# Kernel optimization log

Measured on AMD Instinct MI355X. Metric: run time of the kernel, lower is better.

## Reference

```python
import jax, jax.numpy as jnp
import numpy as np

B, CF, CG, CI = 2, 64, 64, 32
D = H = W = 64

def setup_inputs() -> dict:
    key = jax.random.key(0)
    k1, k2, k3, k4, k5 = jax.random.split(key, 5)
    x = jax.random.normal(k1, (B, CF, D, H, W), dtype=jnp.float32)
    g = jax.random.normal(k2, (B, CG, D, H, W), dtype=jnp.float32)
    # 1x1x1 conv weights reduce to [out_ch, in_ch]; kaiming-like scale
    Wg = jax.random.normal(k3, (CI, CG), dtype=jnp.float32) * (1.0 / np.sqrt(CG))
    Wx = jax.random.normal(k4, (CI, CF), dtype=jnp.float32) * (1.0 / np.sqrt(CF))
    Wpsi = jax.random.normal(k5, (1, CI), dtype=jnp.float32) * (1.0 / np.sqrt(CI))
    return {"x": x, "g": g, "Wg": Wg, "Wx": Wx, "Wpsi": Wpsi}

def reference(x, g, Wg, Wx, Wpsi):
    # 1x1x1 Conv3d == per-voxel matmul over channel dim
    g1 = jnp.einsum('oc,bcdhw->bodhw', Wg, g)          # [B,CI,D,H,W]
    x1 = jnp.einsum('oc,bcdhw->bodhw', Wx, x)          # [B,CI,D,H,W]
    a = jax.nn.relu(g1 + x1)
    psi = jnp.einsum('oc,bcdhw->bodhw', Wpsi, a)       # [B,1,D,H,W]
    psi = jax.nn.sigmoid(psi)
    return x * psi                                      # broadcast over CF
```

## Files before the change

kernel.cpp:

```cpp
#include <hip/hip_runtime.h>


#define SPAT 262144
#define NVOX 524288
#define CIN  64
#define COUT 32

__global__ __launch_bounds__(256) void transpose_w(const float* __restrict__ Wg,
                                                   const float* __restrict__ Wx,
                                                   float* __restrict__ Wcat) {
    int idx = blockIdx.x * 256 + threadIdx.x;
    int c = idx >> 6;
    int o = idx & 63;
    float v = (o < 32) ? Wg[o * CIN + c] : Wx[(o - 32) * CIN + c];
    Wcat[c * 64 + o] = v;
}

__global__ __launch_bounds__(256) void gate_main(const float* __restrict__ x,
                                                 const float* __restrict__ g,
                                                 const float* __restrict__ Wcat,
                                                 const float* __restrict__ Wpsi,
                                                 float* __restrict__ out) {
    int v = blockIdx.x * 256 + threadIdx.x;
    int b = v >> 18;
    int s = v & (SPAT - 1);

    const float* __restrict__ xp = x + (size_t)b * CIN * SPAT + s;
    const float* __restrict__ gp = g + (size_t)b * CIN * SPAT + s;

    float acc[COUT];
#pragma unroll
    for (int o = 0; o < COUT; ++o) acc[o] = 0.0f;

#pragma unroll 4
    for (int c = 0; c < CIN; ++c) {
        float gc = gp[(size_t)c * SPAT];
        float xc = xp[(size_t)c * SPAT];
        const float* w = Wcat + c * 64;
#pragma unroll
        for (int o = 0; o < COUT; ++o)
            acc[o] = fmaf(w[o], gc, fmaf(w[32 + o], xc, acc[o]));
    }

    float p = 0.0f;
#pragma unroll
    for (int o = 0; o < COUT; ++o)
        p = fmaf(Wpsi[o], fmaxf(acc[o], 0.0f), p);

    float psi = 1.0f / (1.0f + __expf(-p));

    float* __restrict__ op = out + (size_t)b * CIN * SPAT + s;
#pragma unroll 4
    for (int c = 0; c < CIN; ++c)
        op[(size_t)c * SPAT] = xp[(size_t)c * SPAT] * psi;
}

extern "C" void kernel_launch(void* const* d_in, const int* in_sizes, int n_in,
                              void* d_out, int out_size, void* d_ws, size_t ws_size,
                              hipStream_t stream) {
    const float* x    = (const float*)d_in[0];
    const float* g    = (const float*)d_in[1];
    const float* Wg   = (const float*)d_in[2];
    const float* Wx   = (const float*)d_in[3];
    const float* Wpsi = (const float*)d_in[4];
    float* out  = (float*)d_out;
    float* Wcat = (float*)d_ws;

    transpose_w<<<16, 256, 0, stream>>>(Wg, Wx, Wcat);
    gate_main<<<NVOX / 256, 256, 0, stream>>>(x, g, Wcat, Wpsi, out);
}
```

Measured before the change: 340.2 us.

## Process two voxels per thread with float2 loads and nontemporal g/out accesses

Each thread now handles two adjacent voxels, using 8-byte vector loads and stores, and reuses each weight load for two voxels. Loads of g and stores of out are marked nontemporal so they do not displace x from cache, since x is re-read in the output pass. Launch bounds request 4 blocks per CU. In exchange each thread holds twice as many accumulators (64 floats), which raises register pressure and may reduce occupancy.

```diff
diff --git a/kernel.cpp b/kernel.cpp
--- a/kernel.cpp
+++ b/kernel.cpp
@@ -5,6 +5,9 @@
 #define NVOX 524288
 #define CIN  64
 #define COUT 32
+#define S2   (SPAT / 2)
+
+typedef float v2f __attribute__((ext_vector_type(2)));
 
 __global__ __launch_bounds__(256) void transpose_w(const float* __restrict__ Wg,
                                                    const float* __restrict__ Wx,
@@ -16,43 +19,52 @@
     Wcat[c * 64 + o] = v;
 }
 
-__global__ __launch_bounds__(256) void gate_main(const float* __restrict__ x,
-                                                 const float* __restrict__ g,
-                                                 const float* __restrict__ Wcat,
-                                                 const float* __restrict__ Wpsi,
-                                                 float* __restrict__ out) {
-    int v = blockIdx.x * 256 + threadIdx.x;
-    int b = v >> 18;
-    int s = v & (SPAT - 1);
+__global__ __launch_bounds__(256, 4) void gate_main(const v2f* __restrict__ x,
+                                                    const v2f* __restrict__ g,
+                                                    const float* __restrict__ Wcat,
+                                                    const float* __restrict__ Wpsi,
+                                                    v2f* __restrict__ out) {
+    int p = blockIdx.x * 256 + threadIdx.x;
+    int b = p >> 17;
+    int s = p & (S2 - 1);
 
-    const float* __restrict__ xp = x + (size_t)b * CIN * SPAT + s;
-    const float* __restrict__ gp = g + (size_t)b * CIN * SPAT + s;
+    const v2f* __restrict__ xp = x + (size_t)b * CIN * S2 + s;
+    const v2f* __restrict__ gp = g + (size_t)b * CIN * S2 + s;
 
-    float acc[COUT];
+    v2f acc[COUT];
 #pragma unroll
-    for (int o = 0; o < COUT; ++o) acc[o] = 0.0f;
+    for (int o = 0; o < COUT; ++o) acc[o] = (v2f)(0.0f);
 
+#pragma unroll 2
+    for (int c = 0; c < CIN; ++c) {
+        v2f gc = __builtin_nontemporal_load(gp + (size_t)c * S2);
+        v2f xc = xp[(size_t)c * S2];
+        const float* w = Wcat + c * 64;
+#pragma unroll
+        for (int o = 0; o < COUT; ++o) {
+            float wg = w[o], wx = w[32 + o];
+            acc[o].x = fmaf(wg, gc.x, fmaf(wx, xc.x, acc[o].x));
+            acc[o].y = fmaf(wg, gc.y, fmaf(wx, xc.y, acc[o].y));
+        }
+    }
+
+    float px = 0.0f, py = 0.0f;
+#pragma unroll
+    for (int o = 0; o < COUT; ++o) {
+        float wp = Wpsi[o];
+        px = fmaf(wp, fmaxf(acc[o].x, 0.0f), px);
+        py = fmaf(wp, fmaxf(acc[o].y, 0.0f), py);
+    }
+    float psix = 1.0f / (1.0f + __expf(-px));
+    float psiy = 1.0f / (1.0f + __expf(-py));
+
+    v2f* __restrict__ op = out + (size_t)b * CIN * S2 + s;
 #pragma unroll 4
     for (int c = 0; c < CIN; ++c) {
-        float gc = gp[(size_t)c * SPAT];
-        float xc = xp[(size_t)c * SPAT];
-        const float* w = Wcat + c * 64;
-#pragma unroll
-        for (int o = 0; o < COUT; ++o)
-            acc[o] = fmaf(w[o], gc, fmaf(w[32 + o], xc, acc[o]));
+        v2f xv = xp[(size_t)c * S2];
+        v2f ov; ov.x = xv.x * psix; ov.y = xv.y * psiy;
+        __builtin_nontemporal_store(ov, op + (size_t)c * S2);
     }
-
-    float p = 0.0f;
-#pragma unroll
-    for (int o = 0; o < COUT; ++o)
-        p = fmaf(Wpsi[o], fmaxf(acc[o], 0.0f), p);
-
-    float psi = 1.0f / (1.0f + __expf(-p));
-
-    float* __restrict__ op = out + (size_t)b * CIN * SPAT + s;
-#pragma unroll 4
-    for (int c = 0; c < CIN; ++c)
-        op[(size_t)c * SPAT] = xp[(size_t)c * SPAT] * psi;
 }
 
 extern "C" void kernel_launch(void* const* d_in, const int* in_sizes, int n_in,
@@ -67,5 +79,6 @@
     float* Wcat = (float*)d_ws;
 
     transpose_w<<<16, 256, 0, stream>>>(Wg, Wx, Wcat);
-    gate_main<<<NVOX / 256, 256, 0, stream>>>(x, g, Wcat, Wpsi, out);
+    gate_main<<<NVOX / 2 / 256, 256, 0, stream>>>((const v2f*)x, (const v2f*)g,
+                                                  Wcat, Wpsi, (v2f*)out);
 }
```

After: 320.8 us. 5.7% less time.
